# Optimization experiments

Hardware: AMD Instinct MI355X
Metric: run time of the kernel (lower is better)

## Reference

```python
import jax, jax.numpy as jnp
import numpy as np

N = 100000   # nodes
E = 500000   # edges
D = 128      # node_hidden_size
ED = 128     # edge_emb_dim
L = 8        # n_message_passes
H = 4        # num_heads
V = 8192     # node_vocab_size
G = 64       # num_graphs
A = 100      # num_actions
NFLOW = 8
NPOS = 64


def setup_inputs() -> dict:
    key = jax.random.key(0)
    ks = jax.random.split(key, 24)
    rn = lambda k, shape, s: jax.random.normal(k, shape, jnp.float32) * s
    inp = {}
    # graph tensors
    inp['x'] = jax.random.randint(ks[0], (N,), 0, V)
    inp['node_type'] = jax.random.randint(ks[1], (N,), 0, 2)
    inp['batch'] = jnp.sort(jax.random.randint(ks[2], (N,), 0, G))
    inp['edge_index'] = jax.random.randint(ks[3], (2, E), 0, N)
    inp['flow'] = jax.random.randint(ks[4], (E,), 0, NFLOW)
    inp['position'] = jax.random.randint(ks[5], (E,), 0, NPOS)
    inp['block'] = jax.random.randint(ks[6], (N,), 0, 4096)
    inp['num_graphs'] = G
    # parameters
    sd = 1.0 / np.sqrt(D)
    se = 1.0 / np.sqrt(ED)
    inp['emb_table'] = rn(ks[7], (V, D), 1.0)
    inp['flow_emb'] = rn(ks[8], (NFLOW, ED), 1.0)
    inp['pos_emb'] = rn(ks[9], (NPOS, ED), 1.0)
    inp['blk_emb'] = rn(ks[10], (2, ED), 1.0)
    inp['Wq'] = rn(ks[11], (L, D, D), sd)
    inp['Wk'] = rn(ks[12], (L, D, D), sd)
    inp['Wv'] = rn(ks[13], (L, D, D), sd)
    inp['Wek'] = rn(ks[14], (L, ED, D), se)
    inp['Wev'] = rn(ks[15], (L, ED, D), se)
    inp['Wo'] = rn(ks[16], (L, D, D), sd)
    inp['Weu'] = rn(ks[17], (L, 2 * D + ED, ED), 1.0 / np.sqrt(2 * D + ED))
    inp['QW1'] = rn(ks[18], (D + ED, D), 1.0 / np.sqrt(D + ED))
    inp['Qb1'] = jnp.zeros((D,), jnp.float32)
    inp['QW2'] = rn(ks[19], (D, A), sd)
    inp['Qb2'] = jnp.zeros((A,), jnp.float32)
    return inp


def _forward(x, node_type, batch, edge_index, flow, position, block, num_graphs,
             emb_table, flow_emb, pos_emb, blk_emb,
             Wq, Wk, Wv, Wek, Wev, Wo, Weu, QW1, Qb1, QW2, Qb2):
    src, dst = edge_index[0], edge_index[1]
    feat = emb_table[x]                                        # [N, D]
    # EdgeEncoding: flow-type + position embeddings + block-crossing indicator
    crossing = (block[src] != block[dst]).astype(jnp.int32)
    e = flow_emb[flow] + pos_emb[position] + blk_emb[crossing]  # [E, ED]

    Nn, Dd = feat.shape
    dh = Dd // H
    scale = 1.0 / np.sqrt(dh)
    n_layers = Wq.shape[0]
    for l in range(n_layers):
        q = (feat @ Wq[l]).reshape(Nn, H, dh)
        k = (feat @ Wk[l]).reshape(Nn, H, dh)
        v = (feat @ Wv[l]).reshape(Nn, H, dh)
        ek = (e @ Wek[l]).reshape(-1, H, dh)
        ev = (e @ Wev[l]).reshape(-1, H, dh)
        # per-edge attention logits, softmax over edges sharing a dst node
        scores = jnp.sum(q[dst] * (k[src] + ek), axis=-1) * scale  # [E, H]
        m = jax.lax.stop_gradient(
            jax.ops.segment_max(scores, dst, num_segments=Nn))
        ex = jnp.exp(scores - m[dst])
        den = jax.ops.segment_sum(ex, dst, num_segments=Nn)
        alpha = ex / (den[dst] + 1e-16)                            # [E, H]
        msg = alpha[..., None] * (v[src] + ev)                     # [E, H, dh]
        agg = jax.ops.segment_sum(msg, dst, num_segments=Nn).reshape(Nn, Dd)
        feat_new = jax.nn.relu(feat + agg @ Wo[l])
        e = jax.nn.relu(e + jnp.concatenate([feat[src], feat[dst], e], axis=-1) @ Weu[l])
        feat = feat_new

    # scatter_mean over instruction nodes (type == 0) per graph
    maskf = (node_type == 0).astype(feat.dtype)
    ncnt = jax.ops.segment_sum(maskf, batch, num_segments=num_graphs)
    gagg = jax.ops.segment_sum(feat * maskf[:, None], batch, num_segments=num_graphs)
    gagg = gagg / jnp.maximum(ncnt, 1.0)[:, None]
    # scatter_mean of edge features per graph (edge's graph = graph of its src node)
    eb = batch[src]
    ecnt = jax.ops.segment_sum(jnp.ones((e.shape[0],), e.dtype), eb, num_segments=num_graphs)
    eagg = jax.ops.segment_sum(e, eb, num_segments=num_graphs)
    eagg = eagg / jnp.maximum(ecnt, 1.0)[:, None]

    ga = jnp.concatenate([gagg, eagg], axis=-1)                    # [G, D+ED]
    h = jax.nn.relu(ga @ QW1 + Qb1)
    logits = h @ QW2 + Qb2
    return jax.nn.log_softmax(logits, axis=-1)


def reference(x, node_type, batch, edge_index, flow, position, block, num_graphs,
              emb_table, flow_emb, pos_emb, blk_emb,
              Wq, Wk, Wv, Wek, Wev, Wo, Weu, QW1, Qb1, QW2, Qb2):
    return _forward(x, node_type, batch, edge_index, flow, position, block,
                    int(num_graphs), emb_table, flow_emb, pos_emb, blk_emb,
                    Wq, Wk, Wv, Wek, Wev, Wo, Weu, QW1, Qb1, QW2, Qb2)
```

## Files before the change

### kernel.cpp

```cpp
#include <hip/hip_runtime.h>
#include <stdint.h>

#define NN 100000
#define NE 500000
#define DD 128
#define NL 8
#define NG 64
#define NA 100
#define DET_PAIRS 65536

typedef unsigned short u16;
typedef unsigned int u32;
typedef __attribute__((ext_vector_type(8))) short short8;
typedef __attribute__((ext_vector_type(4))) float f32x4;

union U4 { uint4 v; u16 s[8]; };

__device__ __forceinline__ float b2f(u16 u){ union{u32 i; float f;} x; x.i=((u32)u)<<16; return x.f; }
__device__ __forceinline__ u16 f2b(float f){ union{float f; u32 i;} x; x.f=f; u32 b=x.i; b += 0x7fffu + ((b>>16)&1u); return (u16)(b>>16); }

__global__ void zero_k(int* __restrict__ p, int n){
  int i = blockIdx.x*256 + threadIdx.x;
  if (i < n) p[i] = 0;
}
__global__ void diag_k(u16* __restrict__ out, int n, float val){
  int i = blockIdx.x*256 + threadIdx.x;
  if (i < n) out[i] = f2b(val);
}

__global__ void detect_k(const u16* __restrict__ raw, int* __restrict__ flags){
  int i = blockIdx.x*256 + threadIdx.x;
  int ok = 0;
  if (i < DET_PAIRS){
    u16 v = raw[2*i];
    int e = (v>>7)&0xFF;
    ok = ((e >= 107 && e <= 147) || ((v & 0x7FFFu) == 0)) ? 1 : 0;
  }
  unsigned long long b = __ballot(ok);
  if ((threadIdx.x & 63) == 0) atomicAdd(&flags[2], (int)__popcll(b));
}
__global__ void flagset_k(int* __restrict__ flags){
  if (threadIdx.x==0) flags[0] = (flags[2] < DET_PAIRS/2) ? 1 : 0;
}
__global__ void tobf16_k(const void* __restrict__ in, u16* __restrict__ out, int n,
                         const int* __restrict__ flags){
  int i = blockIdx.x*256 + threadIdx.x;
  if (i >= n) return;
  if (flags[0]) out[i] = f2b(((const float*)in)[i]);
  else          out[i] = ((const u16*)in)[i];
}
__global__ void convT_k(const void* __restrict__ in, u16* __restrict__ out, int L, int K, int Nn,
                        const int* __restrict__ flags){
  int id = blockIdx.x*256 + threadIdx.x;
  int tot = L*K*Nn;
  if (id >= tot) return;
  int l = id/(K*Nn); int r = id - l*K*Nn;
  int k = r/Nn; int n = r - k*Nn;
  u16 v;
  if (flags[0]) v = f2b(((const float*)in)[id]);
  else          v = ((const u16*)in)[id];
  out[(size_t)l*K*Nn + (size_t)n*K + k] = v;
}

__global__ void featinit_k(const int* __restrict__ x, const u16* __restrict__ emb, u16* __restrict__ feat){
  int id = blockIdx.x*256 + threadIdx.x;
  if (id >= NN*16) return;
  int row = id>>4, c8 = (id&15)*8;
  int g = x[row];
  *(uint4*)(feat + (size_t)row*DD + c8) = *(const uint4*)(emb + (size_t)g*DD + c8);
}

__global__ void count_k(const int* __restrict__ dst, int* __restrict__ cnt){
  int e = blockIdx.x*256 + threadIdx.x;
  if (e < NE) atomicAdd(&cnt[dst[e]], 1);
}
__global__ void scan1_k(const int* __restrict__ cnt, int* __restrict__ excl, int* __restrict__ bsum, int n){
  __shared__ int sh[256];
  int t = threadIdx.x, g = blockIdx.x*256 + t;
  int v = (g<n) ? cnt[g] : 0;
  sh[t] = v; __syncthreads();
  for (int d=1; d<256; d<<=1){
    int xv = (t>=d) ? sh[t-d] : 0;
    __syncthreads();
    sh[t] += xv;
    __syncthreads();
  }
  if (g<n) excl[g] = sh[t]-v;
  if (t==255) bsum[blockIdx.x] = sh[255];
}
__global__ void scan2_k(int* __restrict__ bsum, int nb){
  if (threadIdx.x==0 && blockIdx.x==0){
    int a=0;
    for (int i=0;i<nb;i++){ int x=bsum[i]; bsum[i]=a; a+=x; }
  }
}
__global__ void scan3_k(const int* __restrict__ excl, const int* __restrict__ bsum,
                        int* __restrict__ offs, int* __restrict__ cursor, int n, int total){
  int g = blockIdx.x*256 + threadIdx.x;
  if (g < n){ int o = excl[g] + bsum[g>>8]; offs[g]=o; cursor[g]=o; }
  if (g==0) offs[n] = total;
}
__global__ void fill_k(const int* __restrict__ dst, int* __restrict__ cursor, int* __restrict__ perm){
  int e = blockIdx.x*256 + threadIdx.x;
  if (e < NE){ int p = atomicAdd(&cursor[dst[e]], 1); perm[p] = e; }
}
__global__ void make_sorted_k(const int* __restrict__ perm, const int* __restrict__ src,
                              const int* __restrict__ dst, int* __restrict__ srcs, int* __restrict__ dsts){
  int i = blockIdx.x*256 + threadIdx.x;
  if (i < NE){ int ed = perm[i]; srcs[i] = src[ed]; dsts[i] = dst[ed]; }
}

__global__ void edgeinit_k(const int* __restrict__ perm, const int* __restrict__ flow,
                           const int* __restrict__ pos, const int* __restrict__ blk,
                           const int* __restrict__ srcs, const int* __restrict__ dsts,
                           const int* __restrict__ batch,
                           const u16* __restrict__ flow_emb, const u16* __restrict__ pos_emb,
                           const u16* __restrict__ blk_emb,
                           u16* __restrict__ e, int* __restrict__ ebgs){
  int id = blockIdx.x*256 + threadIdx.x;
  if (id >= NE*16) return;
  int i = id>>4, c8 = (id&15)*8;
  int ed = perm[i];
  int s = srcs[i], d = dsts[i];
  int cross = (blk[s] != blk[d]) ? 1 : 0;
  U4 a,b,c,o;
  a.v = *(const uint4*)(flow_emb + (size_t)flow[ed]*DD + c8);
  b.v = *(const uint4*)(pos_emb  + (size_t)pos[ed]*DD + c8);
  c.v = *(const uint4*)(blk_emb  + (size_t)cross*DD + c8);
  #pragma unroll
  for (int j=0;j<8;j++) o.s[j] = f2b(b2f(a.s[j]) + b2f(b.s[j]) + b2f(c.s[j]));
  *(uint4*)(e + (size_t)i*DD + c8) = o.v;
  if ((id&15)==0) ebgs[i] = batch[s];
}

__global__ __launch_bounds__(256,2) void gemm_k(
    const u16* A0, const int* __restrict__ i0,
    const u16* A1, const int* __restrict__ i1,
    const u16* A2, const int* __restrict__ i2, int nchunks,
    const u16* __restrict__ Bt, int Ktot,
    const u16* res, int do_relu,
    u16* C, int M)
{
  __shared__ u16 As[128*128];
  __shared__ u16 Bs[128*128];
  int t = threadIdx.x;
  int mbase = blockIdx.x*128;
  int lane = t & 63, w = t>>6;
  int wrow = (w>>1)*64, wcol = (w&1)*64;
  f32x4 acc[4][4];
  #pragma unroll
  for (int mi=0;mi<4;mi++)
    #pragma unroll
    for (int ni=0;ni<4;ni++){ acc[mi][ni][0]=0.f; acc[mi][ni][1]=0.f; acc[mi][ni][2]=0.f; acc[mi][ni][3]=0.f; }

  int rl_w = t>>4;
  int gw = t&15;

  for (int c=0; c<nchunks; c++){
    const u16* A = (c==0)?A0:((c==1)?A1:A2);
    const int* idx = (c==0)?i0:((c==1)?i1:i2);
    #pragma unroll
    for (int i=0;i<8;i++){
      int r = rl_w + 16*i;
      int gm = mbase + r;
      uint4 av = make_uint4(0u,0u,0u,0u);
      if (gm < M){
        size_t grow = idx ? (size_t)idx[gm] : (size_t)gm;
        av = *(const uint4*)(A + grow*DD + gw*8);
      }
      *(uint4*)(As + ((size_t)i*256 + gw*16 + rl_w)*8) = av;
      uint4 bv = *(const uint4*)(Bt + (size_t)r*Ktot + c*128 + gw*8);
      *(uint4*)(Bs + ((size_t)i*256 + gw*16 + rl_w)*8) = bv;
    }
    __syncthreads();
    int l15 = lane & 15, quad = lane>>4;
    #pragma unroll
    for (int kk=0;kk<4;kk++){
      short8 af[4], bfr[4];
      #pragma unroll
      for (int mi=0;mi<4;mi++){
        int tileR = (wrow>>4) + mi;
        af[mi] = *(const short8*)(As + ((size_t)tileR*256 + kk*64 + quad*16 + l15)*8);
      }
      #pragma unroll
      for (int ni=0;ni<4;ni++){
        int tileN = (wcol>>4) + ni;
        bfr[ni] = *(const short8*)(Bs + ((size_t)tileN*256 + kk*64 + quad*16 + l15)*8);
      }
      #pragma unroll
      for (int mi=0;mi<4;mi++)
        #pragma unroll
        for (int ni=0;ni<4;ni++)
          acc[mi][ni] = __builtin_amdgcn_mfma_f32_16x16x32_bf16(af[mi], bfr[ni], acc[mi][ni], 0, 0, 0);
    }
    __syncthreads();
  }

  int l15 = lane & 15, quad = lane>>4;
  #pragma unroll
  for (int mi=0;mi<4;mi++){
    #pragma unroll
    for (int r4=0;r4<4;r4++){
      int row = wrow + mi*16 + quad*4 + r4;
      int gm = mbase + row;
      if (gm >= M) continue;
      #pragma unroll
      for (int ni=0;ni<4;ni++){
        int col = wcol + ni*16 + l15;
        float v = acc[mi][ni][r4];
        if (res) v += b2f(res[(size_t)gm*DD + col]);
        if (do_relu && v < 0.f) v = 0.f;
        C[(size_t)gm*DD + col] = f2b(v);
      }
    }
  }
}

__global__ __launch_bounds__(256,2) void scores_fused_k(
    const u16* __restrict__ E, const u16* __restrict__ WekT,
    const u16* __restrict__ q, const u16* __restrict__ k,
    const int* __restrict__ srcs, const int* __restrict__ dsts,
    float* __restrict__ sc)
{
  __shared__ u16 As[128*128];
  __shared__ u16 Bs[128*128];
  int t = threadIdx.x;
  int ebase = blockIdx.x*128;
  int lane = t & 63, w = t>>6;
  int wrow = (w>>1)*64, wcol = (w&1)*64;
  int rl_w = t>>4, gw = t&15;
  #pragma unroll
  for (int i=0;i<8;i++){
    int r = rl_w + 16*i;
    int gm = ebase + r;
    uint4 av = make_uint4(0u,0u,0u,0u);
    if (gm < NE) av = *(const uint4*)(E + (size_t)gm*DD + gw*8);
    *(uint4*)(As + ((size_t)i*256 + gw*16 + rl_w)*8) = av;
    uint4 bv = *(const uint4*)(WekT + (size_t)r*DD + gw*8);
    *(uint4*)(Bs + ((size_t)i*256 + gw*16 + rl_w)*8) = bv;
  }
  __syncthreads();
  int l15 = lane & 15, quad = lane>>4;
  f32x4 acc[4][4];
  #pragma unroll
  for (int mi=0;mi<4;mi++)
    #pragma unroll
    for (int ni=0;ni<4;ni++){ acc[mi][ni][0]=0.f; acc[mi][ni][1]=0.f; acc[mi][ni][2]=0.f; acc[mi][ni][3]=0.f; }
  #pragma unroll
  for (int kk=0;kk<4;kk++){
    short8 af[4], bfr[4];
    #pragma unroll
    for (int mi=0;mi<4;mi++)
      af[mi] = *(const short8*)(As + ((size_t)((wrow>>4)+mi)*256 + kk*64 + quad*16 + l15)*8);
    #pragma unroll
    for (int ni=0;ni<4;ni++)
      bfr[ni] = *(const short8*)(Bs + ((size_t)((wcol>>4)+ni)*256 + kk*64 + quad*16 + l15)*8);
    #pragma unroll
    for (int mi=0;mi<4;mi++)
      #pragma unroll
      for (int ni=0;ni<4;ni++)
        acc[mi][ni] = __builtin_amdgcn_mfma_f32_16x16x32_bf16(af[mi], bfr[ni], acc[mi][ni], 0, 0, 0);
  }
  __syncthreads();
  #pragma unroll
  for (int mi=0;mi<4;mi++){
    #pragma unroll
    for (int r4=0;r4<4;r4++){
      int row = wrow + mi*16 + quad*4 + r4;
      #pragma unroll
      for (int ni=0;ni<4;ni++){
        int col = wcol + ni*16 + l15;
        As[row*128 + ((((col>>3) ^ (row&15))<<3)) + (col&7)] = f2b(acc[mi][ni][r4]);
      }
    }
  }
  __syncthreads();
  const float scale = 0.17677669529663689f;
  for (int pid = t; pid < 512; pid += 256){
    int le = pid>>2, h = pid&3;
    int e = ebase + le;
    if (e >= NE) continue;
    int s = srcs[e], d = dsts[e];
    float dot = 0.f;
    #pragma unroll
    for (int j4=0;j4<4;j4++){
      int off = h*32 + j4*8;
      U4 qv, kv, ev;
      qv.v = *(const uint4*)(q + (size_t)d*DD + off);
      kv.v = *(const uint4*)(k + (size_t)s*DD + off);
      ev.v = *(const uint4*)(As + le*128 + ((((h*4+j4) ^ (le&15))<<3)));
      #pragma unroll
      for (int j=0;j<8;j++) dot += b2f(qv.s[j]) * (b2f(kv.s[j]) + b2f(ev.s[j]));
    }
    sc[(size_t)e*4 + h] = dot * scale;
  }
}

__global__ __launch_bounds__(256,2) void nodeagg_k(
    const float* __restrict__ sc, const u16* __restrict__ v,
    const u16* __restrict__ E, const int* __restrict__ srcs,
    const int* __restrict__ offs, const u16* __restrict__ WevL,
    u16* __restrict__ agg)
{
  __shared__ float sh[16*4*129];
  int t = threadIdx.x;
  int node = blockIdx.x*16 + (t>>4);
  int sub = t & 15, h = sub>>2, p4 = sub&3;
  float uh[32];
  #pragma unroll
  for (int j=0;j<32;j++) uh[j]=0.f;
  float accv[8] = {0.f,0.f,0.f,0.f,0.f,0.f,0.f,0.f};
  int beg = 0, end = 0;
  if (node < NN){ beg = offs[node]; end = offs[node+1]; }
  float m = -1e30f, den = 0.f;
  for (int i=beg;i<end;i++){
    float s = sc[(size_t)i*4 + h];
    float mn = fmaxf(m, s);
    den = den*__expf(m-mn) + __expf(s-mn);
    m = mn;
  }
  float inv = 1.0f/(den + 1e-16f);
  int offv = h*32 + p4*8;
  for (int i=beg;i<end;i++){
    float a = __expf(sc[(size_t)i*4 + h] - m)*inv;
    U4 vv; vv.v = *(const uint4*)(v + (size_t)srcs[i]*DD + offv);
    #pragma unroll
    for (int j=0;j<8;j++) accv[j] += a*b2f(vv.s[j]);
    const u16* er = E + (size_t)i*DD + p4*32;
    #pragma unroll
    for (int qq=0;qq<4;qq++){
      U4 ee; ee.v = *(const uint4*)(er + qq*8);
      #pragma unroll
      for (int j=0;j<8;j++) uh[qq*8+j] += a*b2f(ee.s[j]);
    }
  }
  int base = ((t>>4)*4 + h)*129;
  #pragma unroll
  for (int j=0;j<32;j++) sh[base + p4*32 + j] = uh[j];
  __syncthreads();
  if (node >= NN) return;
  float o8[8];
  #pragma unroll
  for (int j=0;j<8;j++) o8[j] = accv[j];
  for (int kk=0;kk<128;kk+=4){
    float u0 = sh[base+kk], u1 = sh[base+kk+1], u2 = sh[base+kk+2], u3 = sh[base+kk+3];
    U4 w0,w1,w2,w3;
    w0.v = *(const uint4*)(WevL + (size_t)kk*DD + offv);
    w1.v = *(const uint4*)(WevL + (size_t)(kk+1)*DD + offv);
    w2.v = *(const uint4*)(WevL + (size_t)(kk+2)*DD + offv);
    w3.v = *(const uint4*)(WevL + (size_t)(kk+3)*DD + offv);
    #pragma unroll
    for (int j=0;j<8;j++)
      o8[j] += u0*b2f(w0.s[j]) + u1*b2f(w1.s[j]) + u2*b2f(w2.s[j]) + u3*b2f(w3.s[j]);
  }
  U4 o;
  #pragma unroll
  for (int j=0;j<8;j++) o.s[j] = f2b(o8[j]);
  *(uint4*)(agg + (size_t)node*DD + offv) = o.v;
}

__global__ void hist_k(const int* __restrict__ gid, const int* __restrict__ mask, int n,
                       int* __restrict__ hist){
  __shared__ int lh[NG];
  int t = threadIdx.x;
  if (t < NG) lh[t]=0;
  __syncthreads();
  int i = blockIdx.x*256 + t;
  if (i < n && (!mask || mask[i]==0)) atomicAdd(&lh[gid[i]], 1);
  __syncthreads();
  if (t < NG && lh[t]) atomicAdd(&hist[t], lh[t]);
}
__global__ void scan64_k(const int* __restrict__ hist, int* __restrict__ base, int* __restrict__ cur){
  if (threadIdx.x==0){
    int a=0;
    for (int g=0; g<NG; g++){ base[g]=a; cur[g]=a; a+=hist[g]; }
    base[NG]=a;
  }
}
__global__ void fillperm_k(const int* __restrict__ gid, const int* __restrict__ mask, int n,
                           int* __restrict__ cur, int* __restrict__ operm){
  __shared__ int lh[NG];
  __shared__ int lb[NG];
  int t = threadIdx.x;
  if (t < NG) lh[t]=0;
  __syncthreads();
  int i = blockIdx.x*256 + t;
  int g=-1, r=0;
  if (i < n && (!mask || mask[i]==0)){ g = gid[i]; r = atomicAdd(&lh[g], 1); }
  __syncthreads();
  if (t < NG && lh[t]) lb[t] = atomicAdd(&cur[t], lh[t]);
  __syncthreads();
  if (g >= 0) operm[lb[g] + r] = i;
}
__global__ __launch_bounds__(256,4) void poolsum_k(
    const u16* __restrict__ feat, const int* __restrict__ operm,
    const int* __restrict__ base, int chunks, float* __restrict__ outsum)
{
  __shared__ float sh[16*128];
  int g = blockIdx.x / chunks, c = blockIdx.x % chunks;
  int beg = base[g], end = base[g+1];
  int len = end - beg;
  int cb = beg + (int)(((long long)len*c)/chunks);
  int ce = beg + (int)(((long long)len*(c+1))/chunks);
  int t = threadIdx.x, grp = t>>4, sub = t&15;
  float acc[8] = {0.f,0.f,0.f,0.f,0.f,0.f,0.f,0.f};
  for (int i = cb+grp; i < ce; i += 16){
    int r = operm[i];
    U4 fv; fv.v = *(const uint4*)(feat + (size_t)r*DD + sub*8);
    #pragma unroll
    for (int j=0;j<8;j++) acc[j] += b2f(fv.s[j]);
  }
  #pragma unroll
  for (int j=0;j<8;j++) sh[grp*128 + sub*8 + j] = acc[j];
  __syncthreads();
  if (t < 128){
    float s = 0.f;
    #pragma unroll
    for (int r=0;r<16;r++) s += sh[r*128 + t];
    if (s != 0.f) atomicAdd(&outsum[g*DD + t], s);
  }
}

__global__ void ganorm_k(const float* __restrict__ gsum, const int* __restrict__ ncnt,
                         const float* __restrict__ esum, const int* __restrict__ ecnt,
                         float* __restrict__ ga){
  int id = blockIdx.x*256 + threadIdx.x;
  if (id >= NG*256) return;
  int g = id>>8, c = id&255;
  float v;
  if (c < 128) v = gsum[g*DD + c] / fmaxf((float)ncnt[g], 1.f);
  else         v = esum[g*DD + (c-128)] / fmaxf((float)ecnt[g], 1.f);
  ga[(size_t)g*256 + c] = v;
}

__global__ void mlp1_k(const float* __restrict__ ga, const u16* __restrict__ QW1,
                       const u16* __restrict__ Qb1, float* __restrict__ h){
  int o = blockIdx.x*256 + threadIdx.x;
  if (o >= NG*DD) return;
  int g = o>>7, j = o&127;
  float s = b2f(Qb1[j]);
  #pragma unroll 4
  for (int kq=0;kq<256;kq++) s += ga[(size_t)g*256 + kq] * b2f(QW1[(size_t)kq*DD + j]);
  h[o] = fmaxf(s, 0.f);
}

__global__ __launch_bounds__(128) void mlp2_k(const float* __restrict__ h, const u16* __restrict__ QW2,
                       const u16* __restrict__ Qb2, void* __restrict__ out, const int* __restrict__ flags){
  __shared__ float lsh[NA];
  __shared__ float red[128];
  int g = blockIdx.x, t = threadIdx.x;
  float s = -1e30f;
  if (t < NA){
    float acc = b2f(Qb2[t]);
    #pragma unroll 4
    for (int kq=0;kq<DD;kq++) acc += h[(size_t)g*DD + kq] * b2f(QW2[(size_t)kq*NA + t]);
    lsh[t] = acc; s = acc;
  }
  red[t] = s; __syncthreads();
  for (int d=64; d>0; d>>=1){ if (t<d) red[t] = fmaxf(red[t], red[t+d]); __syncthreads(); }
  float m = red[0]; __syncthreads();
  float ex = (t < NA) ? __expf(lsh[t]-m) : 0.f;
  red[t] = ex; __syncthreads();
  for (int d=64; d>0; d>>=1){ if (t<d) red[t] += red[t+d]; __syncthreads(); }
  float lse = m + __logf(red[0]);
  if (t < NA){
    float r = lsh[t]-lse;
    if (flags[0]) ((float*)out)[(size_t)g*NA + t] = r;
    else          ((u16*)out)[(size_t)g*NA + t]  = f2b(r);
  }
}

extern "C" void kernel_launch(void* const* d_in, const int* in_sizes, int n_in,
                              void* d_out, int out_size, void* d_ws, size_t ws_size,
                              hipStream_t stream) {
  (void)in_sizes; (void)n_in;
  const int* x      = (const int*)d_in[0];
  const int* ntype  = (const int*)d_in[1];
  const int* batch  = (const int*)d_in[2];
  const int* eidx   = (const int*)d_in[3];
  const int* src    = eidx;
  const int* dstp   = eidx + NE;
  const int* flow   = (const int*)d_in[4];
  const int* pos    = (const int*)d_in[5];
  const int* blk    = (const int*)d_in[6];

  char* p = (char*)d_ws;
  auto alloc = [&](size_t bytes)->char* {
    char* r = p; p += (bytes + 255) & ~(size_t)255; return r;
  };
  u16* embB  = (u16*)alloc((size_t)8192*DD*2);
  u16* flowB = (u16*)alloc(8*DD*2);
  u16* posB  = (u16*)alloc(64*DD*2);
  u16* blkB  = (u16*)alloc(2*DD*2);
  const size_t WSZb = (size_t)NL*DD*DD*2;
  u16* WevB = (u16*)alloc(WSZb);
  u16* QW1B = (u16*)alloc((size_t)256*DD*2);
  u16* Qb1B = (u16*)alloc(DD*2);
  u16* QW2B = (u16*)alloc((size_t)DD*NA*2);
  u16* Qb2B = (u16*)alloc(NA*2);
  u16* WqT  = (u16*)alloc(WSZb);
  u16* WkT  = (u16*)alloc(WSZb);
  u16* WvT  = (u16*)alloc(WSZb);
  u16* WekT = (u16*)alloc(WSZb);
  u16* WoT  = (u16*)alloc(WSZb);
  u16* WeuT = (u16*)alloc((size_t)NL*DD*384*2);
  const size_t NB = (size_t)NN*DD*2;
  u16* A  = (u16*)alloc(NB);
  u16* QB = (u16*)alloc(NB);
  u16* KB = (u16*)alloc(NB);
  const size_t EB = (size_t)NE*DD*2;
  u16* E = (u16*)alloc(EB);
  float* scores = (float*)alloc((size_t)NE*4*4);
  int* srcs   = (int*)alloc((size_t)NE*4);
  int* dsts   = (int*)alloc((size_t)NE*4);
  int* ebgs   = (int*)alloc((size_t)NE*4);
  int* cnt    = (int*)alloc((size_t)NN*4);
  int* excl   = (int*)alloc((size_t)NN*4);
  int* bsum   = (int*)alloc(1024*4);
  int* offs   = (int*)alloc((size_t)(NN+1)*4);
  int* cursor = (int*)alloc((size_t)NN*4);
  int* perm   = (int*)alloc((size_t)NE*4);
  int* eperm  = (int*)alloc((size_t)NE*4);
  int* nperm  = (int*)alloc((size_t)NN*4);
  int* ehist  = (int*)alloc(NG*4);
  int* ebase  = (int*)alloc((NG+1)*4);
  int* ecur   = (int*)alloc(NG*4);
  int* nhist  = (int*)alloc(NG*4);
  int* nbase  = (int*)alloc((NG+1)*4);
  int* ncur   = (int*)alloc(NG*4);
  float* gsum = (float*)alloc((size_t)NG*DD*4);
  float* esum = (float*)alloc((size_t)NG*DD*4);
  float* ga = (float*)alloc((size_t)NG*256*4);
  float* h  = (float*)alloc((size_t)NG*DD*4);
  int* flags = (int*)alloc(16);

  size_t needed = (size_t)(p - (char*)d_ws);
  if (needed > ws_size){
    diag_k<<<(out_size+255)/256,256,0,stream>>>((u16*)d_out, out_size, (float)(ws_size>>20));
    return;
  }

  zero_k<<<1,256,0,stream>>>(flags, 4);
  detect_k<<<(DET_PAIRS+255)/256,256,0,stream>>>((const u16*)d_in[8], flags);
  flagset_k<<<1,64,0,stream>>>(flags);
  auto conv = [&](int idx, u16* dst, int n){
    tobf16_k<<<(n+255)/256,256,0,stream>>>(d_in[idx], dst, n, flags);
  };
  auto convT = [&](int idx, u16* dst, int L, int K, int Nc){
    int n = L*K*Nc;
    convT_k<<<(n+255)/256,256,0,stream>>>(d_in[idx], dst, L, K, Nc, flags);
  };
  conv(8,  embB,  8192*DD);
  conv(9,  flowB, 8*DD);
  conv(10, posB,  64*DD);
  conv(11, blkB,  2*DD);
  convT(12, WqT,  NL, DD, DD);
  convT(13, WkT,  NL, DD, DD);
  convT(14, WvT,  NL, DD, DD);
  convT(15, WekT, NL, DD, DD);
  conv(16, WevB, NL*DD*DD);
  convT(17, WoT,  NL, DD, DD);
  convT(18, WeuT, NL, 384, DD);
  conv(19, QW1B, 256*DD);
  conv(20, Qb1B, DD);
  conv(21, QW2B, DD*NA);
  conv(22, Qb2B, NA);

  zero_k<<<(NN+255)/256,256,0,stream>>>(cnt, NN);
  count_k<<<(NE+255)/256,256,0,stream>>>(dstp, cnt);
  int nb = (NN+255)/256;
  scan1_k<<<nb,256,0,stream>>>(cnt, excl, bsum, NN);
  scan2_k<<<1,64,0,stream>>>(bsum, nb);
  scan3_k<<<nb,256,0,stream>>>(excl, bsum, offs, cursor, NN, NE);
  fill_k<<<(NE+255)/256,256,0,stream>>>(dstp, cursor, perm);
  make_sorted_k<<<(NE+255)/256,256,0,stream>>>(perm, src, dstp, srcs, dsts);
  featinit_k<<<(NN*16+255)/256,256,0,stream>>>(x, embB, A);
  edgeinit_k<<<(NE*16+255)/256,256,0,stream>>>(perm, flow, pos, blk, srcs, dsts, batch,
                                               flowB, posB, blkB, E, ebgs);

  dim3 gN((NN+127)/128), gE((NE+127)/128);
  for (int l=0; l<NL; l++){
    const u16* wq  = WqT  + (size_t)l*DD*DD;
    const u16* wk  = WkT  + (size_t)l*DD*DD;
    const u16* wv  = WvT  + (size_t)l*DD*DD;
    const u16* wek = WekT + (size_t)l*DD*DD;
    const u16* wo  = WoT  + (size_t)l*DD*DD;
    const u16* wevL= WevB + (size_t)l*DD*DD;
    const u16* weu = WeuT + (size_t)l*DD*384;

    gemm_k<<<gN,256,0,stream>>>(A,nullptr,nullptr,nullptr,nullptr,nullptr,1, wq,128, nullptr,0, QB, NN);
    gemm_k<<<gN,256,0,stream>>>(A,nullptr,nullptr,nullptr,nullptr,nullptr,1, wk,128, nullptr,0, KB, NN);
    scores_fused_k<<<gE,256,0,stream>>>(E, wek, QB, KB, srcs, dsts, scores);
    gemm_k<<<gN,256,0,stream>>>(A,nullptr,nullptr,nullptr,nullptr,nullptr,1, wv,128, nullptr,0, KB, NN);
    nodeagg_k<<<(NN+15)/16,256,0,stream>>>(scores, KB, E, srcs, offs, wevL, QB);
    gemm_k<<<gE,256,0,stream>>>(A,srcs, A,dsts, E,nullptr, 3, weu,384, E,1, E, NE);
    gemm_k<<<gN,256,0,stream>>>(QB,nullptr,nullptr,nullptr,nullptr,nullptr,1, wo,128, A,1, A, NN);
  }

  zero_k<<<1,256,0,stream>>>(ehist, NG);
  zero_k<<<1,256,0,stream>>>(nhist, NG);
  zero_k<<<(NG*DD*2+255)/256,256,0,stream>>>((int*)gsum, NG*DD);
  zero_k<<<(NG*DD*2+255)/256,256,0,stream>>>((int*)esum, NG*DD);
  hist_k<<<(NE+255)/256,256,0,stream>>>(ebgs, nullptr, NE, ehist);
  hist_k<<<(NN+255)/256,256,0,stream>>>(batch, ntype, NN, nhist);
  scan64_k<<<1,64,0,stream>>>(ehist, ebase, ecur);
  scan64_k<<<1,64,0,stream>>>(nhist, nbase, ncur);
  fillperm_k<<<(NE+255)/256,256,0,stream>>>(ebgs, nullptr, NE, ecur, eperm);
  fillperm_k<<<(NN+255)/256,256,0,stream>>>(batch, ntype, NN, ncur, nperm);
  const int ECH = 16, NCH = 4;
  poolsum_k<<<NG*ECH,256,0,stream>>>(E, eperm, ebase, ECH, esum);
  poolsum_k<<<NG*NCH,256,0,stream>>>(A, nperm, nbase, NCH, gsum);
  ganorm_k<<<(NG*256+255)/256,256,0,stream>>>(gsum, nhist, esum, ehist, ga);
  mlp1_k<<<(NG*DD+255)/256,256,0,stream>>>(ga, QW1B, Qb1B, h);
  mlp2_k<<<NG,128,0,stream>>>(h, QW2B, Qb2B, d_out, flags);
}
```

Before: 4.996 ms.

## Factor edge-update GEMM into per-node projections gathered in epilogue; swizzle LDS

```diff
diff --git a/kernel.cpp b/kernel.cpp
--- a/kernel.cpp
+++ b/kernel.cpp
@@ -134,11 +134,11 @@
 }
 
 __global__ __launch_bounds__(256,2) void gemm_k(
-    const u16* A0, const int* __restrict__ i0,
-    const u16* A1, const int* __restrict__ i1,
-    const u16* A2, const int* __restrict__ i2, int nchunks,
+    const u16* A, const int* __restrict__ idx,
     const u16* __restrict__ Bt, int Ktot,
     const u16* res, int do_relu,
+    const u16* __restrict__ g0, const int* __restrict__ gi0,
+    const u16* __restrict__ g1, const int* __restrict__ gi1,
     u16* C, int M)
 {
   __shared__ u16 As[128*128];
@@ -147,56 +147,44 @@
   int mbase = blockIdx.x*128;
   int lane = t & 63, w = t>>6;
   int wrow = (w>>1)*64, wcol = (w&1)*64;
+  int rl_w = t>>4, gw = t&15;
+  #pragma unroll
+  for (int i=0;i<8;i++){
+    int r = rl_w + 16*i;
+    int gm = mbase + r;
+    uint4 av = make_uint4(0u,0u,0u,0u);
+    if (gm < M){
+      size_t grow = idx ? (size_t)idx[gm] : (size_t)gm;
+      av = *(const uint4*)(A + grow*DD + gw*8);
+    }
+    int gid = i*256 + rl_w*16 + (gw ^ rl_w);
+    *(uint4*)(As + (size_t)gid*8) = av;
+    uint4 bv = *(const uint4*)(Bt + (size_t)r*Ktot + gw*8);
+    *(uint4*)(Bs + (size_t)gid*8) = bv;
+  }
+  __syncthreads();
+  int l15 = lane & 15, quad = lane>>4;
   f32x4 acc[4][4];
   #pragma unroll
   for (int mi=0;mi<4;mi++)
     #pragma unroll
     for (int ni=0;ni<4;ni++){ acc[mi][ni][0]=0.f; acc[mi][ni][1]=0.f; acc[mi][ni][2]=0.f; acc[mi][ni][3]=0.f; }
-
-  int rl_w = t>>4;
-  int gw = t&15;
-
-  for (int c=0; c<nchunks; c++){
-    const u16* A = (c==0)?A0:((c==1)?A1:A2);
-    const int* idx = (c==0)?i0:((c==1)?i1:i2);
-    #pragma unroll
-    for (int i=0;i<8;i++){
-      int r = rl_w + 16*i;
-      int gm = mbase + r;
-      uint4 av = make_uint4(0u,0u,0u,0u);
-      if (gm < M){
-        size_t grow = idx ? (size_t)idx[gm] : (size_t)gm;
-        av = *(const uint4*)(A + grow*DD + gw*8);
-      }
-      *(uint4*)(As + ((size_t)i*256 + gw*16 + rl_w)*8) = av;
-      uint4 bv = *(const uint4*)(Bt + (size_t)r*Ktot + c*128 + gw*8);
-      *(uint4*)(Bs + ((size_t)i*256 + gw*16 + rl_w)*8) = bv;
-    }
-    __syncthreads();
-    int l15 = lane & 15, quad = lane>>4;
-    #pragma unroll
-    for (int kk=0;kk<4;kk++){
-      short8 af[4], bfr[4];
+  #pragma unroll
+  for (int kk=0;kk<4;kk++){
+    int kg = kk*4 + quad;
+    short8 af[4], bfr[4];
+    #pragma unroll
+    for (int mi=0;mi<4;mi++)
+      af[mi] = *(const short8*)(As + (size_t)(((wrow>>4)+mi)*256 + l15*16 + (kg ^ l15))*8);
+    #pragma unroll
+    for (int ni=0;ni<4;ni++)
+      bfr[ni] = *(const short8*)(Bs + (size_t)(((wcol>>4)+ni)*256 + l15*16 + (kg ^ l15))*8);
+    #pragma unroll
+    for (int mi=0;mi<4;mi++)
       #pragma unroll
-      for (int mi=0;mi<4;mi++){
-        int tileR = (wrow>>4) + mi;
-        af[mi] = *(const short8*)(As + ((size_t)tileR*256 + kk*64 + quad*16 + l15)*8);
-      }
-      #pragma unroll
-      for (int ni=0;ni<4;ni++){
-        int tileN = (wcol>>4) + ni;
-        bfr[ni] = *(const short8*)(Bs + ((size_t)tileN*256 + kk*64 + quad*16 + l15)*8);
-      }
-      #pragma unroll
-      for (int mi=0;mi<4;mi++)
-        #pragma unroll
-        for (int ni=0;ni<4;ni++)
-          acc[mi][ni] = __builtin_amdgcn_mfma_f32_16x16x32_bf16(af[mi], bfr[ni], acc[mi][ni], 0, 0, 0);
-    }
-    __syncthreads();
-  }
-
-  int l15 = lane & 15, quad = lane>>4;
+      for (int ni=0;ni<4;ni++)
+        acc[mi][ni] = __builtin_amdgcn_mfma_f32_16x16x32_bf16(af[mi], bfr[ni], acc[mi][ni], 0, 0, 0);
+  }
   #pragma unroll
   for (int mi=0;mi<4;mi++){
     #pragma unroll
@@ -204,11 +192,14 @@
       int row = wrow + mi*16 + quad*4 + r4;
       int gm = mbase + row;
       if (gm >= M) continue;
+      int s0 = gi0 ? gi0[gm] : 0;
+      int s1 = gi1 ? gi1[gm] : 0;
       #pragma unroll
       for (int ni=0;ni<4;ni++){
         int col = wcol + ni*16 + l15;
         float v = acc[mi][ni][r4];
         if (res) v += b2f(res[(size_t)gm*DD + col]);
+        if (g0)  v += b2f(g0[(size_t)s0*DD + col]) + b2f(g1[(size_t)s1*DD + col]);
         if (do_relu && v < 0.f) v = 0.f;
         C[(size_t)gm*DD + col] = f2b(v);
       }
@@ -235,9 +226,10 @@
     int gm = ebase + r;
     uint4 av = make_uint4(0u,0u,0u,0u);
     if (gm < NE) av = *(const uint4*)(E + (size_t)gm*DD + gw*8);
-    *(uint4*)(As + ((size_t)i*256 + gw*16 + rl_w)*8) = av;
+    int gid = i*256 + rl_w*16 + (gw ^ rl_w);
+    *(uint4*)(As + (size_t)gid*8) = av;
     uint4 bv = *(const uint4*)(WekT + (size_t)r*DD + gw*8);
-    *(uint4*)(Bs + ((size_t)i*256 + gw*16 + rl_w)*8) = bv;
+    *(uint4*)(Bs + (size_t)gid*8) = bv;
   }
   __syncthreads();
   int l15 = lane & 15, quad = lane>>4;
@@ -248,13 +240,14 @@
     for (int ni=0;ni<4;ni++){ acc[mi][ni][0]=0.f; acc[mi][ni][1]=0.f; acc[mi][ni][2]=0.f; acc[mi][ni][3]=0.f; }
   #pragma unroll
   for (int kk=0;kk<4;kk++){
+    int kg = kk*4 + quad;
     short8 af[4], bfr[4];
     #pragma unroll
     for (int mi=0;mi<4;mi++)
-      af[mi] = *(const short8*)(As + ((size_t)((wrow>>4)+mi)*256 + kk*64 + quad*16 + l15)*8);
+      af[mi] = *(const short8*)(As + (size_t)(((wrow>>4)+mi)*256 + l15*16 + (kg ^ l15))*8);
     #pragma unroll
     for (int ni=0;ni<4;ni++)
-      bfr[ni] = *(const short8*)(Bs + ((size_t)((wcol>>4)+ni)*256 + kk*64 + quad*16 + l15)*8);
+      bfr[ni] = *(const short8*)(Bs + (size_t)(((wcol>>4)+ni)*256 + l15*16 + (kg ^ l15))*8);
     #pragma unroll
     for (int mi=0;mi<4;mi++)
       #pragma unroll
@@ -508,31 +501,37 @@
   u16* A  = (u16*)alloc(NB);
   u16* QB = (u16*)alloc(NB);
   u16* KB = (u16*)alloc(NB);
+  u16* P1 = (u16*)alloc(NB);
   const size_t EB = (size_t)NE*DD*2;
   u16* E = (u16*)alloc(EB);
   float* scores = (float*)alloc((size_t)NE*4*4);
   int* srcs   = (int*)alloc((size_t)NE*4);
   int* dsts   = (int*)alloc((size_t)NE*4);
   int* ebgs   = (int*)alloc((size_t)NE*4);
-  int* cnt    = (int*)alloc((size_t)NN*4);
-  int* excl   = (int*)alloc((size_t)NN*4);
-  int* bsum   = (int*)alloc(1024*4);
   int* offs   = (int*)alloc((size_t)(NN+1)*4);
-  int* cursor = (int*)alloc((size_t)NN*4);
-  int* perm   = (int*)alloc((size_t)NE*4);
-  int* eperm  = (int*)alloc((size_t)NE*4);
-  int* nperm  = (int*)alloc((size_t)NN*4);
-  int* ehist  = (int*)alloc(NG*4);
-  int* ebase  = (int*)alloc((NG+1)*4);
-  int* ecur   = (int*)alloc(NG*4);
-  int* nhist  = (int*)alloc(NG*4);
-  int* nbase  = (int*)alloc((NG+1)*4);
-  int* ncur   = (int*)alloc(NG*4);
   float* gsum = (float*)alloc((size_t)NG*DD*4);
   float* esum = (float*)alloc((size_t)NG*DD*4);
   float* ga = (float*)alloc((size_t)NG*256*4);
   float* h  = (float*)alloc((size_t)NG*DD*4);
   int* flags = (int*)alloc(16);
+
+  char* q = (char*)P1;
+  auto suballoc = [&](size_t bytes)->char* {
+    char* r = q; q += (bytes + 255) & ~(size_t)255; return r;
+  };
+  int* perm   = (int*)suballoc((size_t)NE*4);
+  int* cnt    = (int*)suballoc((size_t)NN*4);
+  int* excl   = (int*)suballoc((size_t)NN*4);
+  int* bsum   = (int*)suballoc(1024*4);
+  int* cursor = (int*)suballoc((size_t)NN*4);
+  int* eperm  = (int*)suballoc((size_t)NE*4);
+  int* nperm  = (int*)suballoc((size_t)NN*4);
+  int* ehist  = (int*)suballoc(NG*4);
+  int* ebase  = (int*)suballoc((NG+1)*4);
+  int* ecur   = (int*)suballoc(NG*4);
+  int* nhist  = (int*)suballoc(NG*4);
+  int* nbase  = (int*)suballoc((NG+1)*4);
+  int* ncur   = (int*)suballoc(NG*4);
 
   size_t needed = (size_t)(p - (char*)d_ws);
   if (needed > ws_size){
@@ -588,19 +587,21 @@
     const u16* wevL= WevB + (size_t)l*DD*DD;
     const u16* weu = WeuT + (size_t)l*DD*384;
 
-    gemm_k<<<gN,256,0,stream>>>(A,nullptr,nullptr,nullptr,nullptr,nullptr,1, wq,128, nullptr,0, QB, NN);
-    gemm_k<<<gN,256,0,stream>>>(A,nullptr,nullptr,nullptr,nullptr,nullptr,1, wk,128, nullptr,0, KB, NN);
+    gemm_k<<<gN,256,0,stream>>>(A,nullptr, wq,128,  nullptr,0, nullptr,nullptr,nullptr,nullptr, QB, NN);
+    gemm_k<<<gN,256,0,stream>>>(A,nullptr, wk,128,  nullptr,0, nullptr,nullptr,nullptr,nullptr, KB, NN);
     scores_fused_k<<<gE,256,0,stream>>>(E, wek, QB, KB, srcs, dsts, scores);
-    gemm_k<<<gN,256,0,stream>>>(A,nullptr,nullptr,nullptr,nullptr,nullptr,1, wv,128, nullptr,0, KB, NN);
+    gemm_k<<<gN,256,0,stream>>>(A,nullptr, wv,128,  nullptr,0, nullptr,nullptr,nullptr,nullptr, KB, NN);
     nodeagg_k<<<(NN+15)/16,256,0,stream>>>(scores, KB, E, srcs, offs, wevL, QB);
-    gemm_k<<<gE,256,0,stream>>>(A,srcs, A,dsts, E,nullptr, 3, weu,384, E,1, E, NE);
-    gemm_k<<<gN,256,0,stream>>>(QB,nullptr,nullptr,nullptr,nullptr,nullptr,1, wo,128, A,1, A, NN);
+    gemm_k<<<gN,256,0,stream>>>(A,nullptr, weu,384,      nullptr,0, nullptr,nullptr,nullptr,nullptr, KB, NN);
+    gemm_k<<<gN,256,0,stream>>>(A,nullptr, weu+128,384,  nullptr,0, nullptr,nullptr,nullptr,nullptr, P1, NN);
+    gemm_k<<<gE,256,0,stream>>>(E,nullptr, weu+256,384,  E,1, KB,srcs, P1,dsts, E, NE);
+    gemm_k<<<gN,256,0,stream>>>(QB,nullptr, wo,128,  A,1, nullptr,nullptr,nullptr,nullptr, A, NN);
   }
 
   zero_k<<<1,256,0,stream>>>(ehist, NG);
   zero_k<<<1,256,0,stream>>>(nhist, NG);
-  zero_k<<<(NG*DD*2+255)/256,256,0,stream>>>((int*)gsum, NG*DD);
-  zero_k<<<(NG*DD*2+255)/256,256,0,stream>>>((int*)esum, NG*DD);
+  zero_k<<<(NG*DD+255)/256,256,0,stream>>>((int*)gsum, NG*DD);
+  zero_k<<<(NG*DD+255)/256,256,0,stream>>>((int*)esum, NG*DD);
   hist_k<<<(NE+255)/256,256,0,stream>>>(ebgs, nullptr, NE, ehist);
   hist_k<<<(NN+255)/256,256,0,stream>>>(batch, ntype, NN, nhist);
   scan64_k<<<1,64,0,stream>>>(ehist, ebase, ecur);
```

Result: slower. 5.889 ms (+17.9%).
